# Kernel optimization log

Measured on AMD Instinct MI355X. Metric: run time of the kernel, lower is better.

The kernel has to match this reference:

```python
import jax, jax.numpy as jnp
import numpy as np


def setup_inputs() -> dict:
    key = jax.random.key(0)
    k1, k2 = jax.random.split(key)
    x = jax.random.normal(k1, (16, 512, 4096), dtype=jnp.float32)      # [N, C_in, L]
    weight = jax.random.normal(k2, (512, 512, 3), dtype=jnp.float32)   # [C_out, C_in, K]
    scale = jnp.ones((1,), dtype=jnp.float32)                           # learned scalar
    return {"x": x, "weight": weight, "scale": scale}


def reference(x, weight, scale):
    EPS = 1e-5
    # per-sample activation scale over (C, L), clamped
    x_scale = jnp.clip(jnp.mean(jnp.abs(x), axis=(1, 2), keepdims=True), EPS)  # [N,1,1]
    x_norm = x / x_scale
    # straight-through binarization: forward sign(w), backward identity
    w_bin = jax.lax.stop_gradient(jnp.sign(weight)) + weight - jax.lax.stop_gradient(weight)
    w_scale = jnp.mean(jnp.abs(weight))  # scalar
    # conv1d, stride=1, padding=1, dilation=1, groups=1  ->  output [N, C_out, L]
    out = jax.lax.conv_general_dilated(
        x_norm, w_bin,
        window_strides=(1,),
        padding=[(1, 1)],
        dimension_numbers=("NCH", "OIH", "NCH"),
    )
    return out * w_scale * x_scale * scale
```

## Files before the change

### kernel.cpp

```cpp
#include <hip/hip_runtime.h>
#include <stdint.h>


#define CIN   512
#define COUT  512
#define LLEN  4096
#define NBAT  16
#define KW    3
#define WELEMS (COUT*CIN*KW)

typedef __bf16 bf16x8 __attribute__((ext_vector_type(8)));
typedef float  f32x4  __attribute__((ext_vector_type(4)));

__device__ __forceinline__ uint32_t f2bf(float f) {
    union { float f; uint32_t u; } v; v.f = f;
    return (v.u + 0x7fffu + ((v.u >> 16) & 1u)) >> 16;
}

__global__ __launch_bounds__(256) void pack_w(const float* __restrict__ w,
                                              unsigned short* __restrict__ wsw,
                                              float* __restrict__ partial) {
    __shared__ float red[256];
    int tid = threadIdx.x;
    int idx = blockIdx.x * 256 + tid;
    float s = 0.f;
    int co = idx >> 9, ci = idx & 511;
#pragma unroll
    for (int t = 0; t < KW; ++t) {
        float v = w[idx * 3 + t];
        s += fabsf(v);
        unsigned short b = (v > 0.f) ? 0x3F80 : ((v < 0.f) ? 0xBF80 : 0);
        wsw[((t * 64 + (ci >> 3)) * 512 + co) * 8 + (ci & 7)] = b;
    }
    red[tid] = s;
    __syncthreads();
    for (int off = 128; off > 0; off >>= 1) {
        if (tid < off) red[tid] += red[tid + off];
        __syncthreads();
    }
    if (tid == 0) partial[blockIdx.x] = red[0];
}

__global__ __launch_bounds__(256) void wscale_final(const float* __restrict__ partial,
                                                    const float* __restrict__ scale,
                                                    float* __restrict__ fac) {
    __shared__ float red[256];
    int tid = threadIdx.x;
    red[tid] = partial[tid] + partial[tid + 256] + partial[tid + 512] + partial[tid + 768];
    __syncthreads();
    for (int off = 128; off > 0; off >>= 1) {
        if (tid < off) red[tid] += red[tid + off];
        __syncthreads();
    }
    if (tid == 0) fac[0] = red[0] * (1.0f / (float)WELEMS) * scale[0];
}

__global__ __launch_bounds__(256, 2) void conv_mfma(const float* __restrict__ x,
                                                    const unsigned short* __restrict__ wsw,
                                                    const float* __restrict__ fac,
                                                    float* __restrict__ out) {
    int swz = (blockIdx.x & 7) * 256 + (blockIdx.x >> 3);
    int cob = swz & 3;
    int lb  = (swz >> 2) & 31;
    int n   = swz >> 7;
    int co0 = cob * 128;
    int l0  = lb * 128;

    __shared__ char Bs[2][8320];

    int tid  = threadIdx.x;
    int wave = tid >> 6;
    int lane = tid & 63;
    int wco  = (wave >> 1) * 64;
    int wl   = (wave & 1) * 64;
    int m    = lane & 15;
    int ks   = lane >> 4;
    const int p  = tid & 15;
    const int fb = tid >> 4;

    const float* xbase = x + (size_t)(n * 512) * LLEN;
    const char*  wb    = (const char*)wsw;

    int aoff[4];
#pragma unroll
    for (int ms = 0; ms < 4; ++ms)
        aoff[ms] = ks * 8192 + (co0 + wco + ms * 16 + m) * 16;

    float4 b0[2], b1[2];
    float  hReg = 0.f;

    auto LOADB = [&](int c) {
        const float* xrow0 = xbase + (size_t)(c * 32 + 2 * p) * LLEN + l0;
        const float* xrow1 = xrow0 + LLEN;
        b0[0] = reinterpret_cast<const float4*>(xrow0)[fb];
        b1[0] = reinterpret_cast<const float4*>(xrow1)[fb];
        b0[1] = reinterpret_cast<const float4*>(xrow0)[fb + 16];
        b1[1] = reinterpret_cast<const float4*>(xrow1)[fb + 16];
        if (tid < 32)
            hReg = (l0 > 0) ? xbase[(size_t)(c * 32 + tid) * LLEN + l0 - 1] : 0.f;
        else if (tid < 64)
            hReg = (l0 + 128 < LLEN) ? xbase[(size_t)(c * 32 + tid - 32) * LLEN + l0 + 128] : 0.f;
    };
    auto WRITEB = [&](char* BsD) {
        int kslot = p >> 2, jj = (2 * p) & 7;
#pragma unroll
        for (int half = 0; half < 2; ++half) {
#pragma unroll
            for (int e = 0; e < 4; ++e) {
                int ll = (fb + half * 16) * 4 + 1 + e;
                uint32_t pk = f2bf(((const float*)&b0[half])[e])
                            | (f2bf(((const float*)&b1[half])[e]) << 16);
                *reinterpret_cast<uint32_t*>(
                    BsD + ll * 64 + ((kslot ^ ((ll >> 1) & 3)) << 4) + jj * 2) = pk;
            }
        }
        if (tid < 32) {
            *reinterpret_cast<unsigned short*>(
                BsD + ((tid >> 3) << 4) + (tid & 7) * 2) = (unsigned short)f2bf(hReg);
        } else if (tid < 64) {
            int ci = tid - 32, ll = 129;
            *reinterpret_cast<unsigned short*>(
                BsD + ll * 64 + (((ci >> 3) ^ ((ll >> 1) & 3)) << 4) + (ci & 7) * 2)
                = (unsigned short)f2bf(hReg);
        }
    };

    f32x4 acc[4][4];
#pragma unroll
    for (int i = 0; i < 4; ++i)
#pragma unroll
        for (int j = 0; j < 4; ++j) acc[i][j] = (f32x4){0.f, 0.f, 0.f, 0.f};

    LOADB(0);
    WRITEB(Bs[0]);
    __syncthreads();

    int cur = 0;
    for (int c = 0; c < 16; ++c) {
        bf16x8 afr[KW][4];
        {
            const char* ab = wb + c * 32768;
#pragma unroll
            for (int t = 0; t < KW; ++t)
#pragma unroll
                for (int ms = 0; ms < 4; ++ms)
                    afr[t][ms] = *reinterpret_cast<const bf16x8*>(
                        ab + t * 524288 + aoff[ms]);
        }
        __builtin_amdgcn_sched_barrier(0);
        if (c < 15) LOADB(c + 1);

        const char* Bc = Bs[cur];
#pragma unroll
        for (int t = 0; t < KW; ++t) {
            bf16x8 bfr[4];
#pragma unroll
            for (int ns = 0; ns < 4; ++ns) {
                int ll = wl + ns * 16 + m + t;
                bfr[ns] = *reinterpret_cast<const bf16x8*>(
                    Bc + ll * 64 + ((ks ^ ((ll >> 1) & 3)) << 4));
            }
#pragma unroll
            for (int ms = 0; ms < 4; ++ms)
#pragma unroll
                for (int ns = 0; ns < 4; ++ns)
                    acc[ms][ns] = __builtin_amdgcn_mfma_f32_16x16x32_bf16(
                        afr[t][ms], bfr[ns], acc[ms][ns], 0, 0, 0);
        }

        if (c < 15) {
            asm volatile("s_waitcnt vmcnt(0)" ::: "memory");
            WRITEB(Bs[cur ^ 1]);
            asm volatile("s_waitcnt lgkmcnt(0)" ::: "memory");
            __builtin_amdgcn_s_barrier();
        }
        cur ^= 1;
    }

    float fscale = fac[0];
    int r4 = (lane >> 4) * 4;
#pragma unroll
    for (int ms = 0; ms < 4; ++ms) {
#pragma unroll
        for (int ns = 0; ns < 4; ++ns) {
            int col  = l0 + wl + ns * 16 + m;
            int row0 = co0 + wco + ms * 16 + r4;
            float* o = out + ((size_t)(n * 512 + row0)) * LLEN + col;
#pragma unroll
            for (int r = 0; r < 4; ++r)
                o[(size_t)r * LLEN] = acc[ms][ns][r] * fscale;
        }
    }
}

extern "C" void kernel_launch(void* const* d_in, const int* in_sizes, int n_in,
                              void* d_out, int out_size, void* d_ws, size_t ws_size,
                              hipStream_t stream) {
    const float* x     = (const float*)d_in[0];
    const float* w     = (const float*)d_in[1];
    const float* scale = (const float*)d_in[2];
    float* out = (float*)d_out;

    float* partials = (float*)d_ws;
    float* fac      = (float*)((char*)d_ws + 4096);
    unsigned short* wsw = (unsigned short*)((char*)d_ws + 8192);

    pack_w<<<(COUT * CIN) / 256, 256, 0, stream>>>(w, wsw, partials);
    wscale_final<<<1, 256, 0, stream>>>(partials, scale, fac);
    conv_mfma<<<NBAT * 4 * 32, 256, 0, stream>>>(x, wsw, fac, out);
}
```

Before: 141.3 us.

## Prefetch weight fragments one chunk ahead with unrolled ping-pong buffers

The main loop is unrolled by two with separate even/odd register sets for weight fragments and two named LDS buffers, so weight fragments for the next chunk are loaded alongside the next activation tile before the current MFMA block runs. Before, the weight loads were issued at the top of each iteration and had to complete before compute. Activation conversion to bf16 now uses the packed v_cvt_pk_bf16_f32 instruction instead of manual rounding. This doubles the A-fragment register footprint, which raises register pressure under the 2-blocks-per-SM launch bound, and it drops the explicit vmcnt wait before the LDS writes, leaving that wait to the compiler.

```diff
diff --git a/kernel.cpp b/kernel.cpp
--- a/kernel.cpp
+++ b/kernel.cpp
@@ -66,7 +66,8 @@
     int co0 = cob * 128;
     int l0  = lb * 128;
 
-    __shared__ char Bs[2][8320];
+    __shared__ char Bs0[8320];
+    __shared__ char Bs1[8320];
 
     int tid  = threadIdx.x;
     int wave = tid >> 6;
@@ -86,9 +87,18 @@
     for (int ms = 0; ms < 4; ++ms)
         aoff[ms] = ks * 8192 + (co0 + wco + ms * 16 + m) * 16;
 
+    bf16x8 aE[KW][4], aO[KW][4];
     float4 b0[2], b1[2];
     float  hReg = 0.f;
 
+    auto LOADA = [&](int c, bf16x8 (&d)[KW][4]) {
+        const char* ab = wb + c * 32768;
+#pragma unroll
+        for (int t = 0; t < KW; ++t)
+#pragma unroll
+            for (int ms = 0; ms < 4; ++ms)
+                d[t][ms] = *reinterpret_cast<const bf16x8*>(ab + t * 524288 + aoff[ms]);
+    };
     auto LOADB = [&](int c) {
         const float* xrow0 = xbase + (size_t)(c * 32 + 2 * p) * LLEN + l0;
         const float* xrow1 = xrow0 + LLEN;
@@ -108,8 +118,10 @@
 #pragma unroll
             for (int e = 0; e < 4; ++e) {
                 int ll = (fb + half * 16) * 4 + 1 + e;
-                uint32_t pk = f2bf(((const float*)&b0[half])[e])
-                            | (f2bf(((const float*)&b1[half])[e]) << 16);
+                float av = ((const float*)&b0[half])[e];
+                float bv = ((const float*)&b1[half])[e];
+                uint32_t pk;
+                asm("v_cvt_pk_bf16_f32 %0, %1, %2" : "=v"(pk) : "v"(av), "v"(bv));
                 *reinterpret_cast<uint32_t*>(
                     BsD + ll * 64 + ((kslot ^ ((ll >> 1) & 3)) << 4) + jj * 2) = pk;
             }
@@ -131,26 +143,7 @@
 #pragma unroll
         for (int j = 0; j < 4; ++j) acc[i][j] = (f32x4){0.f, 0.f, 0.f, 0.f};
 
-    LOADB(0);
-    WRITEB(Bs[0]);
-    __syncthreads();
-
-    int cur = 0;
-    for (int c = 0; c < 16; ++c) {
-        bf16x8 afr[KW][4];
-        {
-            const char* ab = wb + c * 32768;
-#pragma unroll
-            for (int t = 0; t < KW; ++t)
-#pragma unroll
-                for (int ms = 0; ms < 4; ++ms)
-                    afr[t][ms] = *reinterpret_cast<const bf16x8*>(
-                        ab + t * 524288 + aoff[ms]);
-        }
-        __builtin_amdgcn_sched_barrier(0);
-        if (c < 15) LOADB(c + 1);
-
-        const char* Bc = Bs[cur];
+    auto COMPUTE = [&](const bf16x8 (&a)[KW][4], const char* Bc) {
 #pragma unroll
         for (int t = 0; t < KW; ++t) {
             bf16x8 bfr[4];
@@ -165,16 +158,34 @@
 #pragma unroll
                 for (int ns = 0; ns < 4; ++ns)
                     acc[ms][ns] = __builtin_amdgcn_mfma_f32_16x16x32_bf16(
-                        afr[t][ms], bfr[ns], acc[ms][ns], 0, 0, 0);
-        }
-
-        if (c < 15) {
-            asm volatile("s_waitcnt vmcnt(0)" ::: "memory");
-            WRITEB(Bs[cur ^ 1]);
+                        a[t][ms], bfr[ns], acc[ms][ns], 0, 0, 0);
+        }
+    };
+
+    LOADB(0);
+    LOADA(0, aE);
+    WRITEB(Bs0);
+    __syncthreads();
+
+    for (int c = 0; c < 16; c += 2) {
+        LOADB(c + 1);
+        LOADA(c + 1, aO);
+        __builtin_amdgcn_sched_barrier(0);
+        COMPUTE(aE, Bs0);
+        WRITEB(Bs1);
+        asm volatile("s_waitcnt lgkmcnt(0)" ::: "memory");
+        __builtin_amdgcn_s_barrier();
+        __builtin_amdgcn_sched_barrier(0);
+
+        if (c + 2 < 16) { LOADB(c + 2); LOADA(c + 2, aE); }
+        __builtin_amdgcn_sched_barrier(0);
+        COMPUTE(aO, Bs1);
+        if (c + 2 < 16) {
+            WRITEB(Bs0);
             asm volatile("s_waitcnt lgkmcnt(0)" ::: "memory");
             __builtin_amdgcn_s_barrier();
-        }
-        cur ^= 1;
+            __builtin_amdgcn_sched_barrier(0);
+        }
     }
 
     float fscale = fac[0];
```

Measured after the change: 185.5 us. 1.31x slower.

## Use 512-thread blocks with 8 waves and per-tap weight fragment loads

Applied to the files above, without the earlier changes.

The conv kernel now runs 512 threads (8 waves) per 128x128 tile, with each wave owning a 64x32 output sub-tile, so there are half as many accumulators and the B-tile staging is split across more threads. Weight fragments are loaded per tap inside the inner loop instead of all upfront, which cuts register pressure so launch bounds can ask for 4 blocks per CU. The explicit vmcnt wait before the shared-memory write is dropped and sched barriers are moved. In exchange, each wave reuses a weight fragment across fewer columns, and global weight loads now sit right before the MFMAs that use them, which may expose their latency.

```diff
diff --git a/kernel.cpp b/kernel.cpp
--- a/kernel.cpp
+++ b/kernel.cpp
@@ -55,7 +55,7 @@
     if (tid == 0) fac[0] = red[0] * (1.0f / (float)WELEMS) * scale[0];
 }
 
-__global__ __launch_bounds__(256, 2) void conv_mfma(const float* __restrict__ x,
+__global__ __launch_bounds__(512, 4) void conv_mfma(const float* __restrict__ x,
                                                     const unsigned short* __restrict__ wsw,
                                                     const float* __restrict__ fac,
                                                     float* __restrict__ out) {
@@ -66,17 +66,18 @@
     int co0 = cob * 128;
     int l0  = lb * 128;
 
-    __shared__ char Bs[2][8320];
+    __shared__ char Bs0[8320];
+    __shared__ char Bs1[8320];
 
     int tid  = threadIdx.x;
     int wave = tid >> 6;
     int lane = tid & 63;
-    int wco  = (wave >> 1) * 64;
-    int wl   = (wave & 1) * 64;
+    int wco  = (wave >> 2) * 64;
+    int wl   = (wave & 3) * 32;
     int m    = lane & 15;
     int ks   = lane >> 4;
     const int p  = tid & 15;
-    const int fb = tid >> 4;
+    const int f  = tid >> 4;
 
     const float* xbase = x + (size_t)(n * 512) * LLEN;
     const char*  wb    = (const char*)wsw;
@@ -86,16 +87,13 @@
     for (int ms = 0; ms < 4; ++ms)
         aoff[ms] = ks * 8192 + (co0 + wco + ms * 16 + m) * 16;
 
-    float4 b0[2], b1[2];
+    float4 b0, b1;
     float  hReg = 0.f;
 
     auto LOADB = [&](int c) {
         const float* xrow0 = xbase + (size_t)(c * 32 + 2 * p) * LLEN + l0;
-        const float* xrow1 = xrow0 + LLEN;
-        b0[0] = reinterpret_cast<const float4*>(xrow0)[fb];
-        b1[0] = reinterpret_cast<const float4*>(xrow1)[fb];
-        b0[1] = reinterpret_cast<const float4*>(xrow0)[fb + 16];
-        b1[1] = reinterpret_cast<const float4*>(xrow1)[fb + 16];
+        b0 = reinterpret_cast<const float4*>(xrow0)[f];
+        b1 = reinterpret_cast<const float4*>(xrow0 + LLEN)[f];
         if (tid < 32)
             hReg = (l0 > 0) ? xbase[(size_t)(c * 32 + tid) * LLEN + l0 - 1] : 0.f;
         else if (tid < 64)
@@ -104,15 +102,12 @@
     auto WRITEB = [&](char* BsD) {
         int kslot = p >> 2, jj = (2 * p) & 7;
 #pragma unroll
-        for (int half = 0; half < 2; ++half) {
-#pragma unroll
-            for (int e = 0; e < 4; ++e) {
-                int ll = (fb + half * 16) * 4 + 1 + e;
-                uint32_t pk = f2bf(((const float*)&b0[half])[e])
-                            | (f2bf(((const float*)&b1[half])[e]) << 16);
-                *reinterpret_cast<uint32_t*>(
-                    BsD + ll * 64 + ((kslot ^ ((ll >> 1) & 3)) << 4) + jj * 2) = pk;
-            }
+        for (int e = 0; e < 4; ++e) {
+            int ll = f * 4 + 1 + e;
+            uint32_t pk = f2bf(((const float*)&b0)[e])
+                        | (f2bf(((const float*)&b1)[e]) << 16);
+            *reinterpret_cast<uint32_t*>(
+                BsD + ll * 64 + ((kslot ^ ((ll >> 1) & 3)) << 4) + jj * 2) = pk;
         }
         if (tid < 32) {
             *reinterpret_cast<unsigned short*>(
@@ -125,37 +120,30 @@
         }
     };
 
-    f32x4 acc[4][4];
+    f32x4 acc[4][2];
 #pragma unroll
     for (int i = 0; i < 4; ++i)
 #pragma unroll
-        for (int j = 0; j < 4; ++j) acc[i][j] = (f32x4){0.f, 0.f, 0.f, 0.f};
+        for (int j = 0; j < 2; ++j) acc[i][j] = (f32x4){0.f, 0.f, 0.f, 0.f};
 
     LOADB(0);
-    WRITEB(Bs[0]);
+    WRITEB(Bs0);
     __syncthreads();
 
-    int cur = 0;
     for (int c = 0; c < 16; ++c) {
-        bf16x8 afr[KW][4];
-        {
-            const char* ab = wb + c * 32768;
-#pragma unroll
-            for (int t = 0; t < KW; ++t)
-#pragma unroll
-                for (int ms = 0; ms < 4; ++ms)
-                    afr[t][ms] = *reinterpret_cast<const bf16x8*>(
-                        ab + t * 524288 + aoff[ms]);
-        }
+        if (c < 15) LOADB(c + 1);
         __builtin_amdgcn_sched_barrier(0);
-        if (c < 15) LOADB(c + 1);
 
-        const char* Bc = Bs[cur];
+        const char* Bc = (c & 1) ? Bs1 : Bs0;
 #pragma unroll
         for (int t = 0; t < KW; ++t) {
-            bf16x8 bfr[4];
+            bf16x8 afr[4], bfr[2];
+            const char* ab = wb + t * 524288 + c * 32768;
 #pragma unroll
-            for (int ns = 0; ns < 4; ++ns) {
+            for (int ms = 0; ms < 4; ++ms)
+                afr[ms] = *reinterpret_cast<const bf16x8*>(ab + aoff[ms]);
+#pragma unroll
+            for (int ns = 0; ns < 2; ++ns) {
                 int ll = wl + ns * 16 + m + t;
                 bfr[ns] = *reinterpret_cast<const bf16x8*>(
                     Bc + ll * 64 + ((ks ^ ((ll >> 1) & 3)) << 4));
@@ -163,26 +151,25 @@
 #pragma unroll
             for (int ms = 0; ms < 4; ++ms)
 #pragma unroll
-                for (int ns = 0; ns < 4; ++ns)
+                for (int ns = 0; ns < 2; ++ns)
                     acc[ms][ns] = __builtin_amdgcn_mfma_f32_16x16x32_bf16(
-                        afr[t][ms], bfr[ns], acc[ms][ns], 0, 0, 0);
+                        afr[ms], bfr[ns], acc[ms][ns], 0, 0, 0);
         }
 
         if (c < 15) {
-            asm volatile("s_waitcnt vmcnt(0)" ::: "memory");
-            WRITEB(Bs[cur ^ 1]);
+            WRITEB((c & 1) ? Bs0 : Bs1);
             asm volatile("s_waitcnt lgkmcnt(0)" ::: "memory");
             __builtin_amdgcn_s_barrier();
+            __builtin_amdgcn_sched_barrier(0);
         }
-        cur ^= 1;
     }
 
     float fscale = fac[0];
-    int r4 = (lane >> 4) * 4;
+    int r4 = ks * 4;
 #pragma unroll
     for (int ms = 0; ms < 4; ++ms) {
 #pragma unroll
-        for (int ns = 0; ns < 4; ++ns) {
+        for (int ns = 0; ns < 2; ++ns) {
             int col  = l0 + wl + ns * 16 + m;
             int row0 = co0 + wco + ms * 16 + r4;
             float* o = out + ((size_t)(n * 512 + row0)) * LLEN + col;
@@ -207,5 +194,5 @@
 
     pack_w<<<(COUT * CIN) / 256, 256, 0, stream>>>(w, wsw, partials);
     wscale_final<<<1, 256, 0, stream>>>(partials, scale, fac);
-    conv_mfma<<<NBAT * 4 * 32, 256, 0, stream>>>(x, wsw, fac, out);
+    conv_mfma<<<NBAT * 4 * 32, 512, 0, stream>>>(x, wsw, fac, out);
 }
```

After: 194.4 us. 37.5% more time.

## Use four LDS buffers and sync once per two input-channel chunks

Applied to the files above, without the earlier changes.

Expands the shared-memory staging buffer from two to four slots and restructures the main loop to process two chunks per iteration. The two next chunks are written to LDS while the current two are computed, so a block barrier is needed only every two chunks. Weight fragments are now loaded per tap inside the compute step rather than all up front, which cuts register pressure but shortens the latency hiding for those global loads. LDS use per block doubles, which may reduce occupancy.

```diff
diff --git a/kernel.cpp b/kernel.cpp
--- a/kernel.cpp
+++ b/kernel.cpp
@@ -66,7 +66,7 @@
     int co0 = cob * 128;
     int l0  = lb * 128;
 
-    __shared__ char Bs[2][8320];
+    __shared__ char Bs[4][8320];
 
     int tid  = threadIdx.x;
     int wave = tid >> 6;
@@ -131,29 +131,15 @@
 #pragma unroll
         for (int j = 0; j < 4; ++j) acc[i][j] = (f32x4){0.f, 0.f, 0.f, 0.f};
 
-    LOADB(0);
-    WRITEB(Bs[0]);
-    __syncthreads();
-
-    int cur = 0;
-    for (int c = 0; c < 16; ++c) {
-        bf16x8 afr[KW][4];
-        {
-            const char* ab = wb + c * 32768;
-#pragma unroll
-            for (int t = 0; t < KW; ++t)
-#pragma unroll
-                for (int ms = 0; ms < 4; ++ms)
-                    afr[t][ms] = *reinterpret_cast<const bf16x8*>(
-                        ab + t * 524288 + aoff[ms]);
-        }
-        __builtin_amdgcn_sched_barrier(0);
-        if (c < 15) LOADB(c + 1);
-
-        const char* Bc = Bs[cur];
+    auto COMPUTE = [&](int c) {
+        const char* Bc = Bs[c & 3];
 #pragma unroll
         for (int t = 0; t < KW; ++t) {
-            bf16x8 bfr[4];
+            bf16x8 afr[4], bfr[4];
+            const char* ab = wb + t * 524288 + c * 32768;
+#pragma unroll
+            for (int ms = 0; ms < 4; ++ms)
+                afr[ms] = *reinterpret_cast<const bf16x8*>(ab + aoff[ms]);
 #pragma unroll
             for (int ns = 0; ns < 4; ++ns) {
                 int ll = wl + ns * 16 + m + t;
@@ -165,16 +151,32 @@
 #pragma unroll
                 for (int ns = 0; ns < 4; ++ns)
                     acc[ms][ns] = __builtin_amdgcn_mfma_f32_16x16x32_bf16(
-                        afr[t][ms], bfr[ns], acc[ms][ns], 0, 0, 0);
-        }
-
-        if (c < 15) {
-            asm volatile("s_waitcnt vmcnt(0)" ::: "memory");
-            WRITEB(Bs[cur ^ 1]);
+                        afr[ms], bfr[ns], acc[ms][ns], 0, 0, 0);
+        }
+    };
+
+    LOADB(0);
+    WRITEB(Bs[0]);
+    LOADB(1);
+    WRITEB(Bs[1]);
+    __syncthreads();
+
+    for (int c = 0; c < 16; c += 2) {
+        if (c + 2 < 16) LOADB(c + 2);
+        __builtin_amdgcn_sched_barrier(0);
+        COMPUTE(c);
+        if (c + 2 < 16) {
+            WRITEB(Bs[(c + 2) & 3]);
+            LOADB(c + 3);
+        }
+        __builtin_amdgcn_sched_barrier(0);
+        COMPUTE(c + 1);
+        if (c + 2 < 16) {
+            WRITEB(Bs[(c + 3) & 3]);
             asm volatile("s_waitcnt lgkmcnt(0)" ::: "memory");
             __builtin_amdgcn_s_barrier();
-        }
-        cur ^= 1;
+            __builtin_amdgcn_sched_barrier(0);
+        }
     }
 
     float fscale = fac[0];
```

New measurement: 220.8 us. +56.2%, slower.
